# Kernel optimization log

Measured on AMD Instinct MI355X. Metric: run time of the kernel, lower is better.

The kernel has to match this reference:

```python
import jax, jax.numpy as jnp
import numpy as np
from math import factorial

ZS = np.array([0, 1])
NZ = 2
N_BASIS = 3
N_CHAN = N_BASIS * N_BASIS
N_RBF = 8
MAX_L = 3
CUTOFF = 5.5
P_CUT = 6
N_NODES = 10000
N_EDGES = 100000


def _lxlylz_list(max_l):
    out = []
    for l in range(max_l + 1):
        for lx in range(l, -1, -1):
            for ly in range(l - lx, -1, -1):
                out.append((lx, ly, l - lx - ly))
    return out

LXLYLZ = np.array(_lxlylz_list(MAX_L), dtype=np.int32)  # [n_ang, 3]; (0,0,0) is index 0
N_ANG = LXLYLZ.shape[0]  # 20 for max_l=3

# nu=2 rotational invariants: for each l>0, monomial indices with lx+ly+lz==l and multinomial prefactors
NU2 = []
for l in range(1, MAX_L + 1):
    idx = [i for i in range(N_ANG) if int(LXLYLZ[i].sum()) == l]
    pref = np.array([factorial(l) / (factorial(int(LXLYLZ[i][0])) * factorial(int(LXLYLZ[i][1])) * factorial(int(LXLYLZ[i][2]))) for i in idx], dtype=np.float32)
    NU2.append((np.array(idx, dtype=np.int32), pref))


def setup_inputs() -> dict:
    key = jax.random.key(0)
    ks = jax.random.split(key, 6)
    positions = jax.random.normal(ks[0], (N_NODES, 3), jnp.float32)
    atomic_numbers = jax.random.randint(ks[1], (N_NODES,), 0, NZ)
    edge_index = jax.random.randint(ks[2], (2, N_EDGES), 0, N_NODES)
    edge_lengths = jax.random.uniform(ks[3], (N_EDGES,), jnp.float32, 0.5, CUTOFF)
    edge_vectors = jax.random.normal(ks[4], (N_EDGES, 3), jnp.float32)
    W_embed = jax.random.normal(ks[5], (NZ, N_BASIS), jnp.float32) / np.sqrt(NZ)
    return dict(positions=positions, atomic_numbers=atomic_numbers, edge_index=edge_index,
                edge_lengths=edge_lengths, edge_vectors=edge_vectors, W_embed=W_embed)


def reference(positions, atomic_numbers, edge_index, edge_lengths, edge_vectors, W_embed):
    n_nodes = positions.shape[0]
    # node one-hot over zs -> linear embedding
    one_hot = (atomic_numbers[:, None] == jnp.asarray(ZS)[None, :]).astype(W_embed.dtype)
    emb = one_hot @ W_embed  # [N, n_basis]
    # directed edge-type encoding: outer product of sender/receiver embeddings
    enc = (emb[edge_index[0]][:, :, None] * emb[edge_index[1]][:, None, :]).reshape(-1, N_CHAN)  # [E, c]
    # Bessel radial basis * polynomial cutoff
    r = edge_lengths
    n = jnp.arange(1, N_RBF + 1, dtype=r.dtype)
    radial = jnp.sqrt(2.0 / CUTOFF) * jnp.sin(n[None, :] * jnp.pi * r[:, None] / CUTOFF) / r[:, None]
    u = r / CUTOFF
    p = P_CUT
    fc = (1.0 - 0.5 * (p + 1) * (p + 2) * u ** p + p * (p + 2) * u ** (p + 1)
          - 0.5 * p * (p + 1) * u ** (p + 2)) * (u < 1.0)
    radial = radial * fc[:, None]  # [E, n_rbf]
    # angular monomials x^lx y^ly z^lz of unit edge vectors
    unit = edge_vectors / jnp.linalg.norm(edge_vectors, axis=-1, keepdims=True)
    ang = jnp.prod(unit[:, None, :] ** jnp.asarray(LXLYLZ)[None, :, :], axis=-1)  # [E, n_ang]
    # fused 3-tensor edge product then scatter-sum to receiver nodes
    edge_attr = jnp.einsum('er,ea,ec->erac', radial, ang, enc)  # [E, n_rbf, n_ang, c]
    A = jax.ops.segment_sum(edge_attr, edge_index[1], num_segments=n_nodes)  # node_feat_A
    # symmetrize to invariants: nu=1 (l=0 monomial) + nu=2 per-l invariants
    feats = [A[:, :, 0:1, :]]
    for idx, pref in NU2:
        sel = A[:, :, jnp.asarray(idx), :]
        feats.append(jnp.sum(jnp.asarray(pref)[None, None, :, None] * sel * sel, axis=2, keepdims=True))
    B = jnp.concatenate(feats, axis=2)  # node_feat_B: [N, n_rbf, 1+max_l, c]
    return B
```

## Files before the change

kernel.cpp:

```cpp
#include <hip/hip_runtime.h>


#define NN    10000
#define NE    100000
#define NRBF  8
#define NANG  20
#define NCHAN 9
#define CAP   64
#define BROW  28
#define INV_CUT  (1.0f/5.5f)
#define PI_F     3.14159265358979323846f
#define RAD_NORM 0.6030226891555273f

__launch_bounds__(256, 4)
__global__ void scatter_k(const int* __restrict__ an, const int* __restrict__ ei,
                          int* __restrict__ cnt, int* __restrict__ lst) {
    int e = blockIdx.x * blockDim.x + threadIdx.x;
    if (e >= NE) return;
    int src = ei[e];
    int dst = ei[NE + e];
    int zs  = an[src];
    int pos = atomicAdd(&cnt[dst], 1);
    if (pos < CAP) lst[dst * CAP + pos] = e | (zs << 20);
}

__launch_bounds__(64, 4)
__global__ void node_k(const int* __restrict__ an, const float* __restrict__ elen,
                       const float* __restrict__ evec, const float* __restrict__ W,
                       const int* __restrict__ cnt, const int* __restrict__ lst,
                       float* __restrict__ out)
{
    __shared__ float sB[CAP * BROW];
    float* sA = sB;

    const int n   = blockIdx.x;
    const int tid = threadIdx.x;

    int deg = cnt[n]; if (deg > CAP) deg = CAP;
    const int zd = an[n];
    const float W0=W[0], W1=W[1], W2=W[2], W3=W[3], W4=W[4], W5=W[5];

    int zsv = 0;
    if (tid < deg) {
        const int v   = lst[n * CAP + tid];
        const int eid = v & 0xFFFFF;
        zsv = v >> 20;

        const float r  = elen[eid];
        const float vx = evec[3*eid+0], vy = evec[3*eid+1], vz = evec[3*eid+2];
        const float inv = rsqrtf(vx*vx + vy*vy + vz*vz);
        const float x = vx*inv, y = vy*inv, z = vz*inv;

        const float u  = r * INV_CUT;
        const float u2 = u*u, u6 = u2*u2*u2;
        const float fc = (u < 1.0f) ? (1.0f - 28.0f*u6 + 48.0f*u6*u - 21.0f*u6*u2)
                                    : 0.0f;
        const float scale = RAD_NORM * fc / r;
        float s1, c1;
        sincosf(PI_F * u, &s1, &c1);
        const float twoc = 2.0f * c1;
        float sp = 0.0f, s = s1;
        float rad[8];
        #pragma unroll
        for (int k = 0; k < 8; ++k) {
            rad[k] = scale * s;
            const float sn = twoc * s - sp;
            sp = s; s = sn;
        }

        const float xx = x*x, xy = x*y, xz = x*z, yy = y*y, yz = y*z, zz = z*z;
        float* B = &sB[tid * BROW];
        *(float4*)&B[0]  = make_float4(rad[0], rad[1], rad[2], rad[3]);
        *(float4*)&B[4]  = make_float4(rad[4], rad[5], rad[6], rad[7]);
        *(float4*)&B[8]  = make_float4(1.0f, x, y, z);
        *(float4*)&B[12] = make_float4(xx, xy, xz, yy);
        *(float4*)&B[16] = make_float4(yz, zz, x*xx, y*xx);
        *(float4*)&B[20] = make_float4(z*xx, x*yy, x*yz, x*zz);
        *(float4*)&B[24] = make_float4(y*yy, z*yy, y*zz, z*zz);
    }
    const unsigned long long zmask = __ballot(zsv != 0);
    __syncthreads();

    const int r0 = tid & 7;
    const int a0 = tid >> 3;
    float s00=0.f, s01=0.f, s02=0.f;
    float s10=0.f, s11=0.f, s12=0.f;

    for (int e = 0; e < deg; ++e) {
        const float* B = &sB[e * BROW];
        const float z1 = (float)((zmask >> e) & 1ULL);
        const float z0 = 1.0f - z1;
        const float rd = B[r0];
        const float v0 = rd * B[8 + a0];
        const float v1 = rd * B[16 + a0];
        s00 = fmaf(v0, z0, s00); s10 = fmaf(v0, z1, s10);
        s01 = fmaf(v1, z0, s01); s11 = fmaf(v1, z1, s11);
        if (tid < 32) {
            const float v2 = rd * B[24 + a0];
            s02 = fmaf(v2, z0, s02); s12 = fmaf(v2, z1, s12);
        }
    }
    __syncthreads();

    const float wd0 = zd ? W3 : W0, wd1 = zd ? W4 : W1, wd2 = zd ? W5 : W2;
    {
        const float t00 = W0*s00 + W3*s10, t01 = W1*s00 + W4*s10, t02 = W2*s00 + W5*s10;
        float* Ap = &sA[r0*180 + a0*9];
        Ap[0]=t00*wd0; Ap[1]=t00*wd1; Ap[2]=t00*wd2;
        Ap[3]=t01*wd0; Ap[4]=t01*wd1; Ap[5]=t01*wd2;
        Ap[6]=t02*wd0; Ap[7]=t02*wd1; Ap[8]=t02*wd2;
    }
    {
        const float t10 = W0*s01 + W3*s11, t11 = W1*s01 + W4*s11, t12 = W2*s01 + W5*s11;
        float* Ap = &sA[r0*180 + (8 + a0)*9];
        Ap[0]=t10*wd0; Ap[1]=t10*wd1; Ap[2]=t10*wd2;
        Ap[3]=t11*wd0; Ap[4]=t11*wd1; Ap[5]=t11*wd2;
        Ap[6]=t12*wd0; Ap[7]=t12*wd1; Ap[8]=t12*wd2;
    }
    if (tid < 32) {
        const float t20 = W0*s02 + W3*s12, t21 = W1*s02 + W4*s12, t22 = W2*s02 + W5*s12;
        float* Ap = &sA[r0*180 + (16 + a0)*9];
        Ap[0]=t20*wd0; Ap[1]=t20*wd1; Ap[2]=t20*wd2;
        Ap[3]=t21*wd0; Ap[4]=t21*wd1; Ap[5]=t21*wd2;
        Ap[6]=t22*wd0; Ap[7]=t22*wd1; Ap[8]=t22*wd2;
    }
    __syncthreads();

    for (int o = tid; o < NRBF*4*NCHAN; o += 64) {
        const int r = o / 36, rem = o - r*36, l = rem / 9, c = rem - (rem/9)*9;
        const float* Ar = &sA[r * 180 + c];
        float val;
        if (l == 0) {
            val = Ar[0];
        } else if (l == 1) {
            const float v1 = Ar[9], v2 = Ar[18], v3 = Ar[27];
            val = v1*v1 + v2*v2 + v3*v3;
        } else if (l == 2) {
            const float v0=Ar[36], v1=Ar[45], v2=Ar[54],
                        v3=Ar[63], v4=Ar[72], v5=Ar[81];
            val = v0*v0 + 2.0f*(v1*v1 + v2*v2 + v4*v4) + v3*v3 + v5*v5;
        } else {
            const float w0=Ar[90],  w1=Ar[99],  w2=Ar[108], w3=Ar[117], w4=Ar[126];
            const float w5=Ar[135], w6=Ar[144], w7=Ar[153], w8=Ar[162], w9=Ar[171];
            val = w0*w0 + w6*w6 + w9*w9
                + 3.0f*(w1*w1 + w2*w2 + w3*w3 + w5*w5 + w7*w7 + w8*w8)
                + 6.0f*w4*w4;
        }
        out[n * (NRBF*4*NCHAN) + o] = val;
    }
}

extern "C" void kernel_launch(void* const* d_in, const int* in_sizes, int n_in,
                              void* d_out, int out_size, void* d_ws, size_t ws_size,
                              hipStream_t stream) {
    const int*   an   = (const int*)d_in[1];
    const int*   ei   = (const int*)d_in[2];
    const float* elen = (const float*)d_in[3];
    const float* evec = (const float*)d_in[4];
    const float* W    = (const float*)d_in[5];
    float* out = (float*)d_out;

    int* cnt = (int*)d_ws;
    int* lst = cnt + NN;

    hipMemsetAsync(cnt, 0, NN * sizeof(int), stream);
    scatter_k<<<(NE + 255)/256, 256, 0, stream>>>(an, ei, cnt, lst);
    node_k<<<NN, 64, 0, stream>>>(an, elen, evec, W, cnt, lst, out);
}
```

Baseline: 90.38 us.

## Pack four nodes per block, one wavefront each, with wave-local LDS sync

Each 256-thread block now handles four nodes, one per 64-lane wavefront, with a private LDS slice per wave. Block-wide __syncthreads is replaced by an s_waitcnt lgkmcnt(0) fence, since all sharing happens inside one wavefront. The edge accumulation loop is also unrolled by two. This aims to cut per-block launch and barrier overhead, at the cost of more LDS per block (about 28KB), which may limit occupancy.

After: 90.50 us. Within noise of the previous version (+0.1%).

```diff
diff --git a/kernel.cpp b/kernel.cpp
--- a/kernel.cpp
+++ b/kernel.cpp
@@ -8,9 +8,12 @@
 #define NCHAN 9
 #define CAP   64
 #define BROW  28
+#define NODES_PER_BLK 4
 #define INV_CUT  (1.0f/5.5f)
 #define PI_F     3.14159265358979323846f
 #define RAD_NORM 0.6030226891555273f
+
+#define WSYNC() asm volatile("s_waitcnt lgkmcnt(0)" ::: "memory")
 
 __launch_bounds__(256, 4)
 __global__ void scatter_k(const int* __restrict__ an, const int* __restrict__ ei,
@@ -24,25 +27,29 @@
     if (pos < CAP) lst[dst * CAP + pos] = e | (zs << 20);
 }
 
-__launch_bounds__(64, 4)
+__launch_bounds__(256, 4)
 __global__ void node_k(const int* __restrict__ an, const float* __restrict__ elen,
                        const float* __restrict__ evec, const float* __restrict__ W,
                        const int* __restrict__ cnt, const int* __restrict__ lst,
                        float* __restrict__ out)
 {
-    __shared__ float sB[CAP * BROW];
-    float* sA = sB;
+    __shared__ float sB[NODES_PER_BLK * CAP * BROW];
 
-    const int n   = blockIdx.x;
-    const int tid = threadIdx.x;
+    const int tid  = threadIdx.x;
+    const int w    = tid >> 6;
+    const int lane = tid & 63;
+    const int n    = blockIdx.x * NODES_PER_BLK + w;
+
+    float* Bw = &sB[w * CAP * BROW];
+    float* sA = Bw;
 
     int deg = cnt[n]; if (deg > CAP) deg = CAP;
     const int zd = an[n];
     const float W0=W[0], W1=W[1], W2=W[2], W3=W[3], W4=W[4], W5=W[5];
 
     int zsv = 0;
-    if (tid < deg) {
-        const int v   = lst[n * CAP + tid];
+    if (lane < deg) {
+        const int v   = lst[n * CAP + lane];
         const int eid = v & 0xFFFFF;
         zsv = v >> 20;
 
@@ -69,7 +76,7 @@
         }
 
         const float xx = x*x, xy = x*y, xz = x*z, yy = y*y, yz = y*z, zz = z*z;
-        float* B = &sB[tid * BROW];
+        float* B = &Bw[lane * BROW];
         *(float4*)&B[0]  = make_float4(rad[0], rad[1], rad[2], rad[3]);
         *(float4*)&B[4]  = make_float4(rad[4], rad[5], rad[6], rad[7]);
         *(float4*)&B[8]  = make_float4(1.0f, x, y, z);
@@ -79,15 +86,35 @@
         *(float4*)&B[24] = make_float4(y*yy, z*yy, y*zz, z*zz);
     }
     const unsigned long long zmask = __ballot(zsv != 0);
-    __syncthreads();
+    WSYNC();
 
-    const int r0 = tid & 7;
-    const int a0 = tid >> 3;
+    const int r0 = lane & 7;
+    const int a0 = lane >> 3;
     float s00=0.f, s01=0.f, s02=0.f;
     float s10=0.f, s11=0.f, s12=0.f;
 
-    for (int e = 0; e < deg; ++e) {
-        const float* B = &sB[e * BROW];
+    int e = 0;
+    for (; e + 1 < deg; e += 2) {
+        const float* Ba = &Bw[e * BROW];
+        const float* Bb = &Bw[(e+1) * BROW];
+        const float z1a = (float)((zmask >> e) & 1ULL);
+        const float z1b = (float)((zmask >> (e+1)) & 1ULL);
+        const float z0a = 1.0f - z1a, z0b = 1.0f - z1b;
+        const float rda = Ba[r0],      rdb = Bb[r0];
+        const float v0a = rda * Ba[8 + a0],  v0b = rdb * Bb[8 + a0];
+        const float v1a = rda * Ba[16 + a0], v1b = rdb * Bb[16 + a0];
+        s00 = fmaf(v0a, z0a, s00); s10 = fmaf(v0a, z1a, s10);
+        s01 = fmaf(v1a, z0a, s01); s11 = fmaf(v1a, z1a, s11);
+        s00 = fmaf(v0b, z0b, s00); s10 = fmaf(v0b, z1b, s10);
+        s01 = fmaf(v1b, z0b, s01); s11 = fmaf(v1b, z1b, s11);
+        if (lane < 32) {
+            const float v2a = rda * Ba[24 + a0], v2b = rdb * Bb[24 + a0];
+            s02 = fmaf(v2a, z0a, s02); s12 = fmaf(v2a, z1a, s12);
+            s02 = fmaf(v2b, z0b, s02); s12 = fmaf(v2b, z1b, s12);
+        }
+    }
+    if (e < deg) {
+        const float* B = &Bw[e * BROW];
         const float z1 = (float)((zmask >> e) & 1ULL);
         const float z0 = 1.0f - z1;
         const float rd = B[r0];
@@ -95,12 +122,12 @@
         const float v1 = rd * B[16 + a0];
         s00 = fmaf(v0, z0, s00); s10 = fmaf(v0, z1, s10);
         s01 = fmaf(v1, z0, s01); s11 = fmaf(v1, z1, s11);
-        if (tid < 32) {
+        if (lane < 32) {
             const float v2 = rd * B[24 + a0];
             s02 = fmaf(v2, z0, s02); s12 = fmaf(v2, z1, s12);
         }
     }
-    __syncthreads();
+    WSYNC();
 
     const float wd0 = zd ? W3 : W0, wd1 = zd ? W4 : W1, wd2 = zd ? W5 : W2;
     {
@@ -117,16 +144,16 @@
         Ap[3]=t11*wd0; Ap[4]=t11*wd1; Ap[5]=t11*wd2;
         Ap[6]=t12*wd0; Ap[7]=t12*wd1; Ap[8]=t12*wd2;
     }
-    if (tid < 32) {
+    if (lane < 32) {
         const float t20 = W0*s02 + W3*s12, t21 = W1*s02 + W4*s12, t22 = W2*s02 + W5*s12;
         float* Ap = &sA[r0*180 + (16 + a0)*9];
         Ap[0]=t20*wd0; Ap[1]=t20*wd1; Ap[2]=t20*wd2;
         Ap[3]=t21*wd0; Ap[4]=t21*wd1; Ap[5]=t21*wd2;
         Ap[6]=t22*wd0; Ap[7]=t22*wd1; Ap[8]=t22*wd2;
     }
-    __syncthreads();
+    WSYNC();
 
-    for (int o = tid; o < NRBF*4*NCHAN; o += 64) {
+    for (int o = lane; o < NRBF*4*NCHAN; o += 64) {
         const int r = o / 36, rem = o - r*36, l = rem / 9, c = rem - (rem/9)*9;
         const float* Ar = &sA[r * 180 + c];
         float val;
@@ -165,5 +192,5 @@
 
     hipMemsetAsync(cnt, 0, NN * sizeof(int), stream);
     scatter_k<<<(NE + 255)/256, 256, 0, stream>>>(an, ei, cnt, lst);
-    node_k<<<NN, 64, 0, stream>>>(an, elen, evec, W, cnt, lst, out);
+    node_k<<<NN / NODES_PER_BLK, 256, 0, stream>>>(an, elen, evec, W, cnt, lst, out);
 }
```
